# Kernel optimization log

Measured on AMD Instinct MI355X. Metric: run time of the kernel, lower is better.

The kernel has to match this reference:

```python
import jax, jax.numpy as jnp
import numpy as np

R, C, B, E, H = 128, 256, 1, 768, 12
DK = E // H

def setup_inputs() -> dict:
    key = jax.random.key(0)
    ks = jax.random.split(key, 5)
    s = 1.0 / np.sqrt(E)
    return {
        "x": jax.random.normal(ks[0], (R, C, B, E), jnp.float32),
        "Wq": jax.random.normal(ks[1], (E, E), jnp.float32) * s,
        "bq": jnp.zeros((E,), jnp.float32),
        "Wk": jax.random.normal(ks[2], (E, E), jnp.float32) * s,
        "bk": jnp.zeros((E,), jnp.float32),
        "Wv": jax.random.normal(ks[3], (E, E), jnp.float32) * s,
        "bv": jnp.zeros((E,), jnp.float32),
        "Wo": jax.random.normal(ks[4], (E, E), jnp.float32) * s,
        "bo": jnp.zeros((E,), jnp.float32),
    }

def reference(x, Wq, bq, Wk, bk, Wv, bv, Wo, bo):
    n_rows, n_cols, batch, emb = x.shape
    scaling = (DK ** -0.5) / jnp.sqrt(jnp.float32(n_rows))
    # projections (torch Linear: x @ W.T + b)
    q = (x @ Wq.T + bq).reshape(n_rows, n_cols, batch, H, DK) * scaling
    k = (x @ Wk.T + bk).reshape(n_rows, n_cols, batch, H, DK)
    v = (x @ Wv.T + bv).reshape(n_rows, n_cols, batch, H, DK)
    # pooled attention logits: sum over rows r -> [H, B, C, C]
    attn = jnp.einsum('rinhd,rjnhd->hnij', q, k)
    probs = jax.nn.softmax(attn, axis=-1)  # single softmax shared across rows
    # context: [R, C, B, H, DK]
    c = jnp.einsum('hnij,rjnhd->rinhd', probs, v).reshape(n_rows, n_cols, batch, emb)
    out = c @ Wo.T + bo
    return out, probs
```

## Files before the change

### kernel.cpp

```cpp
#include <hip/hip_runtime.h>
#include <math.h>

#define R_  128
#define C_  256
#define E_  768
#define H_  12
#define DK_ 64
#define T_  (R_*C_)
#define RS_ 8
#define LP  40

typedef __attribute__((ext_vector_type(8))) short          bf16x8;
typedef __attribute__((ext_vector_type(4))) float          f32x4;
typedef __attribute__((ext_vector_type(4))) unsigned short u16x4;
typedef __attribute__((ext_vector_type(8))) unsigned short u16x8;

struct HL { unsigned short h, l; };

__device__ __forceinline__ HL split2(float f) {
    HL o;
    unsigned int u = __float_as_uint(f);
    o.h = (unsigned short)(u >> 16);
    float r = f - __uint_as_float(u & 0xFFFF0000u);
    o.l = (unsigned short)(__float_as_uint(r) >> 16);
    return o;
}

__device__ __forceinline__ void gload16(const void* g, void* l) {
    __builtin_amdgcn_global_load_lds(
        (const __attribute__((address_space(1))) unsigned int*)g,
        (__attribute__((address_space(3))) unsigned int*)l,
        16, 0, 0);
}

#define WAIT_VM8()   asm volatile("s_waitcnt vmcnt(8)"   ::: "memory")
#define WAIT_VM0()   asm volatile("s_waitcnt vmcnt(0)"   ::: "memory")
#define WAIT_LGKM0() asm volatile("s_waitcnt lgkmcnt(0)" ::: "memory")
#define SBAR()       __builtin_amdgcn_s_barrier()

__global__ __launch_bounds__(256) void split_kernel(
    const float* __restrict__ src,
    unsigned short* __restrict__ h, unsigned short* __restrict__ l)
{
    const size_t i = ((size_t)blockIdx.x * 256 + threadIdx.x) * 8;
    float4 f0 = *(const float4*)(src + i);
    float4 f1 = *(const float4*)(src + i + 4);
    float v[8] = { f0.x, f0.y, f0.z, f0.w, f1.x, f1.y, f1.z, f1.w };
    u16x8 hh, ll;
    #pragma unroll
    for (int j = 0; j < 8; ++j) { HL e = split2(v[j]); hh[j] = e.h; ll[j] = e.l; }
    *(u16x8*)(h + i) = hh;
    *(u16x8*)(l + i) = ll;
}

template<int OMODE>
__global__ __launch_bounds__(256, 2) void gemm_kernel(
    const unsigned short* __restrict__ Ah, const unsigned short* __restrict__ Al,
    const unsigned short* __restrict__ Bh, const unsigned short* __restrict__ Bl,
    const float* __restrict__ bias, float scale,
    float* __restrict__ Y32, unsigned short* __restrict__ Yh, unsigned short* __restrict__ Yl)
{
    __shared__ __align__(16) unsigned short smem[2][16384];

    const int tid  = threadIdx.x;
    const int m0   = blockIdx.x * 128;
    const int n0   = blockIdx.y * 128;
    const int wave = tid >> 6, lane = tid & 63;
    const int wm   = (wave & 1) * 64, wn = (wave >> 1) * 64;
    const int fr   = lane & 15;
    const int kqs  = (((lane >> 4) ^ ((fr >> 1) & 3)) * 8);

    const int lrow = lane >> 2;
    const int gd   = (lane & 3) ^ ((lane >> 3) & 3);
    const unsigned short* gsrc = (wave == 0) ? Ah : (wave == 1) ? Al
                               : (wave == 2) ? Bh : Bl;
    const int rbase = (wave < 2) ? m0 : n0;
    const unsigned short* sp = gsrc + (size_t)(rbase + lrow) * E_ + 8 * gd;
    const int ltoff = wave * 4096;

    f32x4 acc[4][4] = {};

    {
        unsigned short* lt0 = &smem[0][ltoff];
        #pragma unroll
        for (int i = 0; i < 8; ++i)
            gload16(sp + (size_t)i * 16 * E_, lt0 + i * 512);
        unsigned short* lt1 = &smem[1][ltoff];
        #pragma unroll
        for (int i = 0; i < 8; ++i)
            gload16(sp + 32 + (size_t)i * 16 * E_, lt1 + i * 512);
    }

    const int NT = E_ / 32;
    for (int t = 0; t < NT; ++t) {
        if (t < NT - 1) { WAIT_VM8(); } else { WAIT_VM0(); }
        SBAR();

        const int cur = t & 1;
        const unsigned short* AsH = smem[cur];
        const unsigned short* AsL = smem[cur] + 4096;
        const unsigned short* BsH = smem[cur] + 8192;
        const unsigned short* BsL = smem[cur] + 12288;

        bf16x8 a_h[4], a_l[4], b_h[4], b_l[4];
        #pragma unroll
        for (int u = 0; u < 4; ++u) {
            a_h[u] = *(const bf16x8*)&AsH[(wm + u * 16 + fr) * 32 + kqs];
            a_l[u] = *(const bf16x8*)&AsL[(wm + u * 16 + fr) * 32 + kqs];
            b_h[u] = *(const bf16x8*)&BsH[(wn + u * 16 + fr) * 32 + kqs];
            b_l[u] = *(const bf16x8*)&BsL[(wn + u * 16 + fr) * 32 + kqs];
        }
        WAIT_LGKM0();
        SBAR();

        if (t + 2 < NT) {
            unsigned short* lt = &smem[cur][ltoff];
            const unsigned short* spn = sp + (t + 2) * 32;
            #pragma unroll
            for (int i = 0; i < 8; ++i)
                gload16(spn + (size_t)i * 16 * E_, lt + i * 512);
        }

        #pragma unroll
        for (int i = 0; i < 4; ++i)
            #pragma unroll
            for (int j = 0; j < 4; ++j) {
                acc[i][j] = __builtin_amdgcn_mfma_f32_16x16x32_bf16(a_h[i], b_h[j], acc[i][j], 0, 0, 0);
                acc[i][j] = __builtin_amdgcn_mfma_f32_16x16x32_bf16(a_h[i], b_l[j], acc[i][j], 0, 0, 0);
                acc[i][j] = __builtin_amdgcn_mfma_f32_16x16x32_bf16(a_l[i], b_h[j], acc[i][j], 0, 0, 0);
            }
    }

    float* rep = (float*)&smem[0][0] + wave * 1024;
    const int mr = lane >> 2;
    const int nc = (lane & 3) * 16;
    #pragma unroll
    for (int ti = 0; ti < 4; ++ti) {
        __syncthreads();
        #pragma unroll
        for (int tj = 0; tj < 4; ++tj)
            #pragma unroll
            for (int r = 0; r < 4; ++r)
                rep[((lane >> 4) * 4 + r) * 64 + tj * 16 + fr] = acc[ti][tj][r];
        __syncthreads();
        float v[16];
        #pragma unroll
        for (int c = 0; c < 4; ++c)
            *(float4*)&v[4 * c] = *(const float4*)&rep[mr * 64 + nc + 4 * c];
        const int gm = m0 + wm + ti * 16 + mr;
        const int gn = n0 + wn + nc;
        if constexpr (OMODE == 1) {
            #pragma unroll
            for (int c = 0; c < 4; ++c) {
                float4 bv = *(const float4*)&bias[gn + 4 * c];
                float4 o;
                o.x = (v[4*c+0] + bv.x) * scale; o.y = (v[4*c+1] + bv.y) * scale;
                o.z = (v[4*c+2] + bv.z) * scale; o.w = (v[4*c+3] + bv.w) * scale;
                *(float4*)&Y32[(size_t)gm * E_ + gn + 4 * c] = o;
            }
        } else {
            unsigned short hh[16], ll[16];
            #pragma unroll
            for (int c = 0; c < 4; ++c) {
                float4 bv = *(const float4*)&bias[gn + 4 * c];
                HL e0 = split2((v[4*c+0] + bv.x) * scale);
                HL e1 = split2((v[4*c+1] + bv.y) * scale);
                HL e2 = split2((v[4*c+2] + bv.z) * scale);
                HL e3 = split2((v[4*c+3] + bv.w) * scale);
                hh[4*c+0] = e0.h; ll[4*c+0] = e0.l;
                hh[4*c+1] = e1.h; ll[4*c+1] = e1.l;
                hh[4*c+2] = e2.h; ll[4*c+2] = e2.l;
                hh[4*c+3] = e3.h; ll[4*c+3] = e3.l;
            }
            u16x8 H0, H1, L0, L1;
            #pragma unroll
            for (int j = 0; j < 8; ++j) { H0[j] = hh[j]; H1[j] = hh[8+j]; L0[j] = ll[j]; L1[j] = ll[8+j]; }
            *(u16x8*)&Yh[(size_t)gm * E_ + gn]     = H0;
            *(u16x8*)&Yh[(size_t)gm * E_ + gn + 8] = H1;
            *(u16x8*)&Yl[(size_t)gm * E_ + gn]     = L0;
            *(u16x8*)&Yl[(size_t)gm * E_ + gn + 8] = L1;
        }
    }
}

__global__ __launch_bounds__(256, 2) void attn_mfma(
    const unsigned short* __restrict__ Qh, const unsigned short* __restrict__ Ql,
    const unsigned short* __restrict__ Kh, const unsigned short* __restrict__ Kl,
    float* __restrict__ part)
{
    __shared__ __align__(16) unsigned short smem[2][16384];

    const int tid  = threadIdx.x;
    const int i0   = blockIdx.x * 128;
    const int j0   = blockIdx.y * 128;
    const int hz   = blockIdx.z;
    const int h    = hz >> 3;
    const int rc   = hz & 7;
    const int wave = tid >> 6, lane = tid & 63;
    const int wm   = (wave & 1) * 64, wn = (wave >> 1) * 64;
    const int fr   = lane & 15;
    const int kqs  = (((lane >> 4) ^ ((fr >> 1) & 3)) * 8);

    const int lrow = lane >> 2;
    const int gd   = (lane & 3) ^ ((lane >> 3) & 3);
    const unsigned short* gsrc = (wave == 0) ? Qh : (wave == 1) ? Ql
                               : (wave == 2) ? Kh : Kl;
    const int rbase = (wave < 2) ? i0 : j0;
    const int ltoff = wave * 4096;
    const unsigned short* sp0 =
        gsrc + ((size_t)(rc * 16 * C_) + rbase + lrow) * E_ + h * DK_ + 8 * gd;

    f32x4 acc[4][4] = {};

    {
        unsigned short* lt0 = &smem[0][ltoff];
        #pragma unroll
        for (int i = 0; i < 8; ++i)
            gload16(sp0 + (size_t)i * 16 * E_, lt0 + i * 512);
        unsigned short* lt1 = &smem[1][ltoff];
        #pragma unroll
        for (int i = 0; i < 8; ++i)
            gload16(sp0 + 32 + (size_t)i * 16 * E_, lt1 + i * 512);
    }

    for (int t = 0; t < 32; ++t) {
        if (t < 31) { WAIT_VM8(); } else { WAIT_VM0(); }
        SBAR();

        const int cur = t & 1;
        const unsigned short* AsH = smem[cur];
        const unsigned short* AsL = smem[cur] + 4096;
        const unsigned short* BsH = smem[cur] + 8192;
        const unsigned short* BsL = smem[cur] + 12288;

        bf16x8 a_h[4], a_l[4], b_h[4], b_l[4];
        #pragma unroll
        for (int u = 0; u < 4; ++u) {
            a_h[u] = *(const bf16x8*)&AsH[(wm + u * 16 + fr) * 32 + kqs];
            a_l[u] = *(const bf16x8*)&AsL[(wm + u * 16 + fr) * 32 + kqs];
            b_h[u] = *(const bf16x8*)&BsH[(wn + u * 16 + fr) * 32 + kqs];
            b_l[u] = *(const bf16x8*)&BsL[(wn + u * 16 + fr) * 32 + kqs];
        }
        WAIT_LGKM0();
        SBAR();

        if (t + 2 < 32) {
            const int sn = t + 2;
            const unsigned short* spn =
                sp0 + (size_t)(sn >> 1) * C_ * E_ + (sn & 1) * 32;
            unsigned short* lt = &smem[cur][ltoff];
            #pragma unroll
            for (int i = 0; i < 8; ++i)
                gload16(spn + (size_t)i * 16 * E_, lt + i * 512);
        }

        #pragma unroll
        for (int i = 0; i < 4; ++i)
            #pragma unroll
            for (int j = 0; j < 4; ++j) {
                acc[i][j] = __builtin_amdgcn_mfma_f32_16x16x32_bf16(a_h[i], b_h[j], acc[i][j], 0, 0, 0);
                acc[i][j] = __builtin_amdgcn_mfma_f32_16x16x32_bf16(a_h[i], b_l[j], acc[i][j], 0, 0, 0);
                acc[i][j] = __builtin_amdgcn_mfma_f32_16x16x32_bf16(a_l[i], b_h[j], acc[i][j], 0, 0, 0);
            }
    }

    float* rep = (float*)&smem[0][0] + wave * 1024;
    const int mr = lane >> 2;
    const int nc = (lane & 3) * 16;
    #pragma unroll
    for (int ti = 0; ti < 4; ++ti) {
        __syncthreads();
        #pragma unroll
        for (int tj = 0; tj < 4; ++tj)
            #pragma unroll
            for (int r = 0; r < 4; ++r)
                rep[((lane >> 4) * 4 + r) * 64 + tj * 16 + fr] = acc[ti][tj][r];
        __syncthreads();
        const int gi = i0 + wm + ti * 16 + mr;
        const int gj = j0 + wn + nc;
        #pragma unroll
        for (int c = 0; c < 4; ++c) {
            float4 o = *(const float4*)&rep[mr * 64 + nc + 4 * c];
            *(float4*)&part[((size_t)(rc * H_ + h) * C_ + gi) * C_ + gj + 4 * c] = o;
        }
    }
}

__global__ __launch_bounds__(256) void softmax_split(
    const float* __restrict__ part, float* __restrict__ probs,
    unsigned short* __restrict__ ph, unsigned short* __restrict__ pl)
{
    const int row = blockIdx.x;
    const int j = threadIdx.x;
    const int wave = j >> 6, lane = j & 63;

    float s = 0.0f;
    #pragma unroll
    for (int rcn = 0; rcn < RS_; ++rcn)
        s += part[((size_t)rcn * H_ * C_ + row) * C_ + j];

    float m = s;
    #pragma unroll
    for (int off = 32; off > 0; off >>= 1)
        m = fmaxf(m, __shfl_down(m, off, 64));
    __shared__ float redm[4];
    if (lane == 0) redm[wave] = m;
    __syncthreads();
    m = fmaxf(fmaxf(redm[0], redm[1]), fmaxf(redm[2], redm[3]));

    float e = expf(s - m);
    float t = e;
    #pragma unroll
    for (int off = 32; off > 0; off >>= 1)
        t += __shfl_down(t, off, 64);
    __shared__ float reds[4];
    if (lane == 0) reds[wave] = t;
    __syncthreads();
    t = reds[0] + reds[1] + reds[2] + reds[3];

    float p = e / t;
    probs[(size_t)row * C_ + j] = p;
    HL sp = split2(p);
    ph[(size_t)row * C_ + j] = sp.h;
    pl[(size_t)row * C_ + j] = sp.l;
}

__global__ __launch_bounds__(256, 2) void ctx_mfma(
    const unsigned short* __restrict__ Ph, const unsigned short* __restrict__ Pl,
    const unsigned short* __restrict__ Vh, const unsigned short* __restrict__ Vl,
    unsigned short* __restrict__ Ch, unsigned short* __restrict__ Cl)
{
    __shared__ __align__(16) unsigned short smem[15360];
    unsigned short* PsH = smem;
    unsigned short* PsL = smem + 5120;
    unsigned short* VsH = smem + 10240;
    unsigned short* VsL = smem + 12800;

    const int tid  = threadIdx.x;
    const int i0   = blockIdx.x * 128;
    const int r    = blockIdx.y;
    const int h    = blockIdx.z;
    const int wave = tid >> 6, lane = tid & 63;
    const int wm   = (wave & 1) * 64, wn = (wave >> 1) * 32;
    const int fr   = lane & 15;
    const int kq   = (lane >> 4) * 8;
    const int srow = tid >> 1;
    const int sk   = (tid & 1) * 16;
    const int vjj  = tid & 31;
    const int vdg  = tid >> 5;

    f32x4 acc[4][2] = {};

    for (int s = 0; s < 8; ++s) {
        const int jb = s * 32;
        const size_t pb = ((size_t)(h * C_) + i0 + srow) * C_ + jb + sk;
        *(u16x8*)&PsH[srow * LP + sk]     = *(const u16x8*)&Ph[pb];
        *(u16x8*)&PsH[srow * LP + sk + 8] = *(const u16x8*)&Ph[pb + 8];
        *(u16x8*)&PsL[srow * LP + sk]     = *(const u16x8*)&Pl[pb];
        *(u16x8*)&PsL[srow * LP + sk + 8] = *(const u16x8*)&Pl[pb + 8];
        const size_t vb = ((size_t)(r * C_) + jb + vjj) * E_ + h * DK_ + vdg * 8;
        u16x8 v_h = *(const u16x8*)&Vh[vb];
        u16x8 v_l = *(const u16x8*)&Vl[vb];
        #pragma unroll
        for (int u = 0; u < 8; ++u) {
            VsH[(vdg * 8 + u) * LP + vjj] = v_h[u];
            VsL[(vdg * 8 + u) * LP + vjj] = v_l[u];
        }
        __syncthreads();

        bf16x8 p_h[4], p_l[4], w_h[2], w_l[2];
        #pragma unroll
        for (int t = 0; t < 4; ++t) {
            p_h[t] = *(const bf16x8*)&PsH[(wm + t * 16 + fr) * LP + kq];
            p_l[t] = *(const bf16x8*)&PsL[(wm + t * 16 + fr) * LP + kq];
        }
        #pragma unroll
        for (int t = 0; t < 2; ++t) {
            w_h[t] = *(const bf16x8*)&VsH[(wn + t * 16 + fr) * LP + kq];
            w_l[t] = *(const bf16x8*)&VsL[(wn + t * 16 + fr) * LP + kq];
        }
        #pragma unroll
        for (int i = 0; i < 4; ++i)
            #pragma unroll
            for (int j = 0; j < 2; ++j) {
                acc[i][j] = __builtin_amdgcn_mfma_f32_16x16x32_bf16(p_h[i], w_h[j], acc[i][j], 0, 0, 0);
                acc[i][j] = __builtin_amdgcn_mfma_f32_16x16x32_bf16(p_h[i], w_l[j], acc[i][j], 0, 0, 0);
                acc[i][j] = __builtin_amdgcn_mfma_f32_16x16x32_bf16(p_l[i], w_h[j], acc[i][j], 0, 0, 0);
            }
        __syncthreads();
    }

    float* rep = (float*)smem + wave * 512;
    const int mr = lane >> 2;
    const int nc = (lane & 3) * 8;
    #pragma unroll
    for (int ti = 0; ti < 4; ++ti) {
        __syncthreads();
        #pragma unroll
        for (int tj = 0; tj < 2; ++tj)
            #pragma unroll
            for (int rr = 0; rr < 4; ++rr)
                rep[((lane >> 4) * 4 + rr) * 32 + tj * 16 + fr] = acc[ti][tj][rr];
        __syncthreads();
        float v[8];
        *(float4*)&v[0] = *(const float4*)&rep[mr * 32 + nc];
        *(float4*)&v[4] = *(const float4*)&rep[mr * 32 + nc + 4];
        const int gm = r * C_ + i0 + wm + ti * 16 + mr;
        const int gn = h * DK_ + wn + nc;
        u16x8 H8, L8;
        #pragma unroll
        for (int jj = 0; jj < 8; ++jj) { HL e = split2(v[jj]); H8[jj] = e.h; L8[jj] = e.l; }
        *(u16x8*)&Ch[(size_t)gm * E_ + gn] = H8;
        *(u16x8*)&Cl[(size_t)gm * E_ + gn] = L8;
    }
}

extern "C" void kernel_launch(void* const* d_in, const int* in_sizes, int n_in,
                              void* d_out, int out_size, void* d_ws, size_t ws_size,
                              hipStream_t stream)
{
    (void)in_sizes; (void)n_in; (void)out_size; (void)ws_size;

    const float* x  = (const float*)d_in[0];
    const float* Wq = (const float*)d_in[1];
    const float* bq = (const float*)d_in[2];
    const float* Wk = (const float*)d_in[3];
    const float* bk = (const float*)d_in[4];
    const float* Wv = (const float*)d_in[5];
    const float* bv = (const float*)d_in[6];
    const float* Wo = (const float*)d_in[7];
    const float* bo = (const float*)d_in[8];

    float* out   = (float*)d_out;
    float* probs = out + (size_t)T_ * E_;
    float* part  = out;

    const size_t QN = (size_t)T_ * E_;
    const size_t WN = (size_t)E_ * E_;
    unsigned short* qh = (unsigned short*)d_ws;
    unsigned short* ql = qh + QN;
    unsigned short* kh = ql + QN;
    unsigned short* kl = kh + QN;
    unsigned short* vh = kl + QN;
    unsigned short* vl = vh + QN;
    unsigned short* ph = kh;
    unsigned short* pl = kh + (size_t)H_ * C_ * C_;
    unsigned short* ch = qh;
    unsigned short* cl = ql;

    unsigned short* xh   = (unsigned short*)out;
    unsigned short* xl   = xh + QN;
    unsigned short* wsph = (unsigned short*)probs;
    unsigned short* wspl = wsph + WN;
    unsigned short* woh  = kl;
    unsigned short* wol  = kl + WN;

    const float scaling = 0.125f / sqrtf(128.0f);

    dim3 blk(256);
    const int xblocks = (int)(QN / 2048);
    const int wblocks = (int)(WN / 2048);

    split_kernel<<<dim3(xblocks), blk, 0, stream>>>(x, xh, xl);

    split_kernel<<<dim3(wblocks), blk, 0, stream>>>(Wq, wsph, wspl);
    gemm_kernel<0><<<dim3(T_ / 128, E_ / 128), blk, 0, stream>>>(
        xh, xl, wsph, wspl, bq, scaling, nullptr, qh, ql);

    split_kernel<<<dim3(wblocks), blk, 0, stream>>>(Wk, wsph, wspl);
    gemm_kernel<0><<<dim3(T_ / 128, E_ / 128), blk, 0, stream>>>(
        xh, xl, wsph, wspl, bk, 1.0f, nullptr, kh, kl);

    split_kernel<<<dim3(wblocks), blk, 0, stream>>>(Wv, wsph, wspl);
    gemm_kernel<0><<<dim3(T_ / 128, E_ / 128), blk, 0, stream>>>(
        xh, xl, wsph, wspl, bv, 1.0f, nullptr, vh, vl);

    attn_mfma<<<dim3(C_ / 128, C_ / 128, H_ * RS_), blk, 0, stream>>>(qh, ql, kh, kl, part);

    split_kernel<<<dim3(wblocks), blk, 0, stream>>>(Wo, woh, wol);

    softmax_split<<<dim3(H_ * C_), blk, 0, stream>>>(part, probs, ph, pl);
    ctx_mfma<<<dim3(C_ / 128, R_, H_), blk, 0, stream>>>(ph, pl, vh, vl, ch, cl);

    gemm_kernel<1><<<dim3(T_ / 128, E_ / 128), blk, 0, stream>>>(
        ch, cl, woh, wol, bo, 1.0f, out, nullptr, nullptr);
}
```

Measured before the change: 922.4 us.

## Load B operand directly from global into registers, halve LDS and raise occupancy

```diff
diff --git a/kernel.cpp b/kernel.cpp
--- a/kernel.cpp
+++ b/kernel.cpp
@@ -33,11 +33,6 @@
         16, 0, 0);
 }
 
-#define WAIT_VM8()   asm volatile("s_waitcnt vmcnt(8)"   ::: "memory")
-#define WAIT_VM0()   asm volatile("s_waitcnt vmcnt(0)"   ::: "memory")
-#define WAIT_LGKM0() asm volatile("s_waitcnt lgkmcnt(0)" ::: "memory")
-#define SBAR()       __builtin_amdgcn_s_barrier()
-
 __global__ __launch_bounds__(256) void split_kernel(
     const float* __restrict__ src,
     unsigned short* __restrict__ h, unsigned short* __restrict__ l)
@@ -54,13 +49,13 @@
 }
 
 template<int OMODE>
-__global__ __launch_bounds__(256, 2) void gemm_kernel(
+__global__ __launch_bounds__(256, 3) void gemm_kernel(
     const unsigned short* __restrict__ Ah, const unsigned short* __restrict__ Al,
     const unsigned short* __restrict__ Bh, const unsigned short* __restrict__ Bl,
     const float* __restrict__ bias, float scale,
     float* __restrict__ Y32, unsigned short* __restrict__ Yh, unsigned short* __restrict__ Yl)
 {
-    __shared__ __align__(16) unsigned short smem[2][16384];
+    __shared__ __align__(16) unsigned short smem[2][8192];
 
     const int tid  = threadIdx.x;
     const int m0   = blockIdx.x * 128;
@@ -68,57 +63,53 @@
     const int wave = tid >> 6, lane = tid & 63;
     const int wm   = (wave & 1) * 64, wn = (wave >> 1) * 64;
     const int fr   = lane & 15;
+    const int kq   = (lane >> 4) * 8;
     const int kqs  = (((lane >> 4) ^ ((fr >> 1) & 3)) * 8);
 
-    const int lrow = lane >> 2;
-    const int gd   = (lane & 3) ^ ((lane >> 3) & 3);
-    const unsigned short* gsrc = (wave == 0) ? Ah : (wave == 1) ? Al
-                               : (wave == 2) ? Bh : Bl;
-    const int rbase = (wave < 2) ? m0 : n0;
-    const unsigned short* sp = gsrc + (size_t)(rbase + lrow) * E_ + 8 * gd;
-    const int ltoff = wave * 4096;
+    const int lrow  = lane >> 2;
+    const int gd    = (lane & 3) ^ ((lane >> 3) & 3);
+    const int rhalf = (wave & 1) * 64;
+    const unsigned short* asrc = ((wave >> 1) ? Al : Ah)
+                                 + (size_t)(m0 + rhalf + lrow) * E_ + 8 * gd;
+    const int ltoff = (wave >> 1) * 4096 + rhalf * 32;
+
+    const unsigned short* bhp = Bh + (size_t)(n0 + wn + fr) * E_ + kq;
+    const unsigned short* blp = Bl + (size_t)(n0 + wn + fr) * E_ + kq;
 
     f32x4 acc[4][4] = {};
 
-    {
-        unsigned short* lt0 = &smem[0][ltoff];
-        #pragma unroll
-        for (int i = 0; i < 8; ++i)
-            gload16(sp + (size_t)i * 16 * E_, lt0 + i * 512);
-        unsigned short* lt1 = &smem[1][ltoff];
-        #pragma unroll
-        for (int i = 0; i < 8; ++i)
-            gload16(sp + 32 + (size_t)i * 16 * E_, lt1 + i * 512);
-    }
+    #pragma unroll
+    for (int i = 0; i < 4; ++i)
+        gload16(asrc + (size_t)i * 16 * E_, &smem[0][ltoff + i * 512]);
 
     const int NT = E_ / 32;
     for (int t = 0; t < NT; ++t) {
-        if (t < NT - 1) { WAIT_VM8(); } else { WAIT_VM0(); }
-        SBAR();
-
+        const int k0  = t * 32;
         const int cur = t & 1;
+        __syncthreads();
+
+        bf16x8 b_h[4], b_l[4];
+        #pragma unroll
+        for (int u = 0; u < 4; ++u) {
+            b_h[u] = *(const bf16x8*)(bhp + k0 + (size_t)u * 16 * E_);
+            b_l[u] = *(const bf16x8*)(blp + k0 + (size_t)u * 16 * E_);
+        }
+        __builtin_amdgcn_sched_barrier(0);
+
+        if (t + 1 < NT) {
+            #pragma unroll
+            for (int i = 0; i < 4; ++i)
+                gload16(asrc + k0 + 32 + (size_t)i * 16 * E_,
+                        &smem[cur ^ 1][ltoff + i * 512]);
+        }
+
         const unsigned short* AsH = smem[cur];
         const unsigned short* AsL = smem[cur] + 4096;
-        const unsigned short* BsH = smem[cur] + 8192;
-        const unsigned short* BsL = smem[cur] + 12288;
-
-        bf16x8 a_h[4], a_l[4], b_h[4], b_l[4];
+        bf16x8 a_h[4], a_l[4];
         #pragma unroll
         for (int u = 0; u < 4; ++u) {
             a_h[u] = *(const bf16x8*)&AsH[(wm + u * 16 + fr) * 32 + kqs];
             a_l[u] = *(const bf16x8*)&AsL[(wm + u * 16 + fr) * 32 + kqs];
-            b_h[u] = *(const bf16x8*)&BsH[(wn + u * 16 + fr) * 32 + kqs];
-            b_l[u] = *(const bf16x8*)&BsL[(wn + u * 16 + fr) * 32 + kqs];
-        }
-        WAIT_LGKM0();
-        SBAR();
-
-        if (t + 2 < NT) {
-            unsigned short* lt = &smem[cur][ltoff];
-            const unsigned short* spn = sp + (t + 2) * 32;
-            #pragma unroll
-            for (int i = 0; i < 8; ++i)
-                gload16(spn + (size_t)i * 16 * E_, lt + i * 512);
         }
 
         #pragma unroll
@@ -188,7 +179,7 @@
     const unsigned short* __restrict__ Kh, const unsigned short* __restrict__ Kl,
     float* __restrict__ part)
 {
-    __shared__ __align__(16) unsigned short smem[2][16384];
+    __shared__ __align__(16) unsigned short smem[2][8192];
 
     const int tid  = threadIdx.x;
     const int i0   = blockIdx.x * 128;
@@ -199,59 +190,55 @@
     const int wave = tid >> 6, lane = tid & 63;
     const int wm   = (wave & 1) * 64, wn = (wave >> 1) * 64;
     const int fr   = lane & 15;
+    const int kq   = (lane >> 4) * 8;
     const int kqs  = (((lane >> 4) ^ ((fr >> 1) & 3)) * 8);
 
-    const int lrow = lane >> 2;
-    const int gd   = (lane & 3) ^ ((lane >> 3) & 3);
-    const unsigned short* gsrc = (wave == 0) ? Qh : (wave == 1) ? Ql
-                               : (wave == 2) ? Kh : Kl;
-    const int rbase = (wave < 2) ? i0 : j0;
-    const int ltoff = wave * 4096;
-    const unsigned short* sp0 =
-        gsrc + ((size_t)(rc * 16 * C_) + rbase + lrow) * E_ + h * DK_ + 8 * gd;
+    const int lrow  = lane >> 2;
+    const int gd    = (lane & 3) ^ ((lane >> 3) & 3);
+    const int rhalf = (wave & 1) * 64;
+    const unsigned short* qsrc = ((wave >> 1) ? Ql : Qh)
+        + ((size_t)(rc * 16 * C_) + i0 + rhalf + lrow) * E_ + h * DK_ + 8 * gd;
+    const int ltoff = (wave >> 1) * 4096 + rhalf * 32;
+
+    const unsigned short* khp = Kh
+        + ((size_t)(rc * 16 * C_) + j0 + wn + fr) * E_ + h * DK_ + kq;
+    const unsigned short* klp = Kl
+        + ((size_t)(rc * 16 * C_) + j0 + wn + fr) * E_ + h * DK_ + kq;
 
     f32x4 acc[4][4] = {};
 
-    {
-        unsigned short* lt0 = &smem[0][ltoff];
-        #pragma unroll
-        for (int i = 0; i < 8; ++i)
-            gload16(sp0 + (size_t)i * 16 * E_, lt0 + i * 512);
-        unsigned short* lt1 = &smem[1][ltoff];
-        #pragma unroll
-        for (int i = 0; i < 8; ++i)
-            gload16(sp0 + 32 + (size_t)i * 16 * E_, lt1 + i * 512);
-    }
+    #pragma unroll
+    for (int i = 0; i < 4; ++i)
+        gload16(qsrc + (size_t)i * 16 * E_, &smem[0][ltoff + i * 512]);
 
     for (int t = 0; t < 32; ++t) {
-        if (t < 31) { WAIT_VM8(); } else { WAIT_VM0(); }
-        SBAR();
-
+        const size_t soff = (size_t)(t >> 1) * C_ * E_ + (t & 1) * 32;
         const int cur = t & 1;
+        __syncthreads();
+
+        bf16x8 b_h[4], b_l[4];
+        #pragma unroll
+        for (int u = 0; u < 4; ++u) {
+            b_h[u] = *(const bf16x8*)(khp + soff + (size_t)u * 16 * E_);
+            b_l[u] = *(const bf16x8*)(klp + soff + (size_t)u * 16 * E_);
+        }
+        __builtin_amdgcn_sched_barrier(0);
+
+        if (t + 1 < 32) {
+            const size_t snoff = (size_t)((t + 1) >> 1) * C_ * E_ + ((t + 1) & 1) * 32;
+            #pragma unroll
+            for (int i = 0; i < 4; ++i)
+                gload16(qsrc + snoff + (size_t)i * 16 * E_,
+                        &smem[cur ^ 1][ltoff + i * 512]);
+        }
+
         const unsigned short* AsH = smem[cur];
         const unsigned short* AsL = smem[cur] + 4096;
-        const unsigned short* BsH = smem[cur] + 8192;
-        const unsigned short* BsL = smem[cur] + 12288;
-
-        bf16x8 a_h[4], a_l[4], b_h[4], b_l[4];
+        bf16x8 a_h[4], a_l[4];
         #pragma unroll
         for (int u = 0; u < 4; ++u) {
             a_h[u] = *(const bf16x8*)&AsH[(wm + u * 16 + fr) * 32 + kqs];
             a_l[u] = *(const bf16x8*)&AsL[(wm + u * 16 + fr) * 32 + kqs];
-            b_h[u] = *(const bf16x8*)&BsH[(wn + u * 16 + fr) * 32 + kqs];
-            b_l[u] = *(const bf16x8*)&BsL[(wn + u * 16 + fr) * 32 + kqs];
-        }
-        WAIT_LGKM0();
-        SBAR();
-
-        if (t + 2 < 32) {
-            const int sn = t + 2;
-            const unsigned short* spn =
-                sp0 + (size_t)(sn >> 1) * C_ * E_ + (sn & 1) * 32;
-            unsigned short* lt = &smem[cur][ltoff];
-            #pragma unroll
-            for (int i = 0; i < 8; ++i)
-                gload16(spn + (size_t)i * 16 * E_, lt + i * 512);
         }
 
         #pragma unroll
```

New measurement: 1.193 ms. 1.29x slower.
